# Performance work log

Hardware: AMD Instinct MI355X
Metric: run time of the kernel (lower is better)

The kernel has to match this reference:

```python
import jax, jax.numpy as jnp
import numpy as np


def setup_inputs() -> dict:
    key = jax.random.key(0)
    ks = jax.random.split(key, 16)
    s = 0.02
    return {
        "video": jax.random.normal(ks[0], (256, 10, 7, 7, 512), jnp.float32),
        "audio": jax.random.normal(ks[1], (10, 256, 128), jnp.float32),
        "Wv1": jax.random.normal(ks[2], (512, 512), jnp.float32) * s,
        "bv1": jnp.zeros((512,), jnp.float32),
        "Wa1": jax.random.normal(ks[3], (512, 128), jnp.float32) * s,
        "ba1": jnp.zeros((512,), jnp.float32),
        "Wb": jax.random.normal(ks[4], (256, 512), jnp.float32) * s,
        "bb": jnp.zeros((256,), jnp.float32),
        "Wc": jax.random.normal(ks[5], (512, 256), jnp.float32) * s,
        "bc": jnp.zeros((512,), jnp.float32),
        "Wv2": jax.random.normal(ks[6], (256, 512), jnp.float32) * s,
        "bv2": jnp.zeros((256,), jnp.float32),
        "Wa2": jax.random.normal(ks[7], (256, 128), jnp.float32) * s,
        "ba2": jnp.zeros((256,), jnp.float32),
        "Ws": jax.random.normal(ks[8], (1, 256), jnp.float32) * s,
        "bs": jnp.zeros((1,), jnp.float32),
    }


def reference(video, audio, Wv1, bv1, Wa1, ba1, Wb, bb, Wc, bc, Wv2, bv2, Wa2, ba2, Ws, bs):
    # video: [B, T, H, W, 512]; audio: [T, B, 128] (transposed inside, as in torch code)
    relu = jax.nn.relu
    audio = jnp.transpose(audio, (1, 0, 2))                  # [B, T, 128]
    B, T, H, W, Vd = video.shape
    BT, HW = B * T, H * W
    af = audio.reshape(BT, -1)                               # [BT, 128]
    vf = video.reshape(B, T, HW, Vd)                         # raw visual feature

    # channel attention
    aq1 = relu(af @ Wa1.T + ba1)[:, None, :]                 # [BT, 1, 512]
    vq1 = relu(vf @ Wv1.T + bv1).reshape(BT, HW, -1)         # [BT, 49, 512]
    avq = jnp.mean(aq1 * vq1, axis=-2)                       # [BT, 512]
    avq = relu(avq @ Wb.T + bb)                              # [BT, 256]
    c_att_maps = jax.nn.sigmoid(avq @ Wc.T + bc).reshape(B, T, 1, Vd)
    c_att = (vf * (c_att_maps + 1.0)).reshape(BT, HW, Vd)    # [BT, 49, 512]

    # spatial attention
    cq = relu(c_att @ Wv2.T + bv2)                           # [BT, 49, 256]
    aq2 = relu(af @ Wa2.T + ba2)[:, None, :]                 # [BT, 1, 256]
    logits = jnp.tanh((cq * aq2) @ Ws.T + bs)                # [BT, 49, 1]
    s_att = jax.nn.softmax(jnp.transpose(logits, (0, 2, 1)), axis=-1)  # [BT, 1, 49]

    out = jnp.matmul(s_att, c_att)                           # [BT, 1, 512]
    return out.reshape(B, T, Vd)
```

## Files before the change

### kernel.cpp

```cpp
#include <hip/hip_runtime.h>

typedef __bf16 bf16x8 __attribute__((ext_vector_type(8)));
typedef float f32x4 __attribute__((ext_vector_type(4)));

__device__ __forceinline__ unsigned short f2bf(float f) {
    union { float f; unsigned int u; } x; x.f = f;
    unsigned int r = x.u + 0x7FFFu + ((x.u >> 16) & 1u);
    return (unsigned short)(r >> 16);
}
__device__ __forceinline__ float bf2f(unsigned short v) {
    union { unsigned int u; float f; } x; x.u = ((unsigned int)v) << 16; return x.f;
}
__device__ __forceinline__ unsigned int cvt_pk_bf16(float lo, float hi) {
    unsigned int r;
    asm("v_cvt_pk_bf16_f32 %0, %1, %2" : "=v"(r) : "v"(lo), "v"(hi));
    return r;
}
__device__ __forceinline__ void async16(const void* g, void* l) {
    __builtin_amdgcn_global_load_lds(
        (const __attribute__((address_space(1))) unsigned int*)g,
        (__attribute__((address_space(3))) unsigned int*)l, 16, 0, 0);
}

__global__ __launch_bounds__(256) void k_front(
    const float* __restrict__ Wv1, const float* __restrict__ Wv2,
    unsigned short* __restrict__ Wv1bf, unsigned short* __restrict__ Wv2bf,
    const float* __restrict__ audio,
    const float* __restrict__ Wa1, const float* __restrict__ ba1,
    const float* __restrict__ Wa2, const float* __restrict__ ba2,
    float* __restrict__ aq1, float* __restrict__ aq2)
{
    const int b = blockIdx.x;
    const int tid = threadIdx.x;
    if (b < 384) {
        int base = b * 1024 + tid;
#pragma unroll
        for (int r = 0; r < 4; ++r) {
            int idx = base + r * 256;
            if (idx < 262144) Wv1bf[idx] = f2bf(Wv1[idx]);
            else              Wv2bf[idx - 262144] = f2bf(Wv2[idx - 262144]);
        }
        return;
    }
    __shared__ float afs[4][128];
    const int btBase = (b - 384) * 4;
    for (int i = tid; i < 512; i += 256) {
        int g = i >> 7, k = i & 127;
        int bt = btBase + g;
        int bb_ = bt / 10, t = bt - bb_ * 10;
        afs[g][k] = audio[(t * 256 + bb_) * 128 + k];
    }
    __syncthreads();
    const int c = tid;
    float a1a[4] = {0.f,0.f,0.f,0.f}, a1b[4] = {0.f,0.f,0.f,0.f}, a2[4] = {0.f,0.f,0.f,0.f};
    const float* w1a = Wa1 + c * 128;
    const float* w1b = Wa1 + (c + 256) * 128;
    const float* w2p = Wa2 + c * 128;
    for (int kk = 0; kk < 32; ++kk) {
        float4 va = *(const float4*)(w1a + kk * 4);
        float4 vb = *(const float4*)(w1b + kk * 4);
        float4 vc = *(const float4*)(w2p + kk * 4);
        float fa[4] = {va.x, va.y, va.z, va.w};
        float fb[4] = {vb.x, vb.y, vb.z, vb.w};
        float fc[4] = {vc.x, vc.y, vc.z, vc.w};
#pragma unroll
        for (int j = 0; j < 4; ++j) {
            int k = kk * 4 + j;
#pragma unroll
            for (int g = 0; g < 4; ++g) {
                float a = afs[g][k];
                a1a[g] += a * fa[j];
                a1b[g] += a * fb[j];
                a2[g]  += a * fc[j];
            }
        }
    }
    float b1a = ba1[c], b1b = ba1[c + 256], b2 = ba2[c];
#pragma unroll
    for (int g = 0; g < 4; ++g) {
        int bt = btBase + g;
        aq1[bt * 512 + c]       = fmaxf(a1a[g] + b1a, 0.f);
        aq1[bt * 512 + c + 256] = fmaxf(a1b[g] + b1b, 0.f);
        aq2[bt * 256 + c]       = fmaxf(a2[g] + b2, 0.f);
    }
}

__global__ __launch_bounds__(512) void k_chanatt_g(
    const float* __restrict__ video,
    const unsigned short* __restrict__ Wv1bf, const float* __restrict__ bv1,
    const float* __restrict__ aq1, float* __restrict__ avq)
{
    __shared__ unsigned short lds[2 * 12288];
    const int tid = threadIdx.x;
    const int wave = tid >> 6, lane = tid & 63, quad = lane >> 4, l16 = lane & 15;
    const int wm = wave >> 2, wn = wave & 3;
    const int mb = blockIdx.x >> 1, nb = blockIdx.x & 1;
    const int bt0 = mb * 2;

    const int arow = tid >> 2, ac = tid & 3;
    const int ahw = arow & 63, abtl = arow >> 6;
    const bool aok = (ahw < 49);
    const int aswz = (ac ^ (arow & 3)) << 3;
    const float* avsrc = video + (size_t)(bt0 + abtl) * 25088 + ahw * 512;
    float4 va, vb;

    auto aload = [&](int kt) {
        if (aok) {
            int k0 = kt * 32 + aswz;
            va = *(const float4*)(avsrc + k0);
            vb = *(const float4*)(avsrc + k0 + 4);
        }
    };
    auto awrite = [&](int buf) {
        if (aok) {
            uint4 o;
            o.x = cvt_pk_bf16(va.x, va.y); o.y = cvt_pk_bf16(va.z, va.w);
            o.z = cvt_pk_bf16(vb.x, vb.y); o.w = cvt_pk_bf16(vb.z, vb.w);
            *(uint4*)&lds[buf * 12288 + tid * 8] = o;
        }
    };
    auto stageB = [&](int buf, int kt) {
#pragma unroll
        for (int rep = 0; rep < 2; ++rep) {
            int q = tid + rep * 512;
            int row = q >> 2, c = q & 3;
            async16(Wv1bf + (size_t)((nb << 8) + row) * 512
                          + kt * 32 + ((c ^ (row & 3)) << 3),
                    &lds[buf * 12288 + 4096 + q * 8]);
        }
    };

    f32x4 acc[4][4];
#pragma unroll
    for (int mt = 0; mt < 4; ++mt)
#pragma unroll
        for (int nt = 0; nt < 4; ++nt)
            acc[mt][nt] = (f32x4){0.f, 0.f, 0.f, 0.f};

    aload(0);
    stageB(0, 0);
    awrite(0);
    __syncthreads();

    for (int kt = 0; kt < 16; ++kt) {
        int cur = kt & 1;
        if (kt < 15) { aload(kt + 1); stageB(cur ^ 1, kt + 1); }
        const int cb = cur * 12288;
        bf16x8 af[4];
#pragma unroll
        for (int mt = 0; mt < 4; ++mt) {
            int row = wm * 64 + mt * 16 + l16;
            af[mt] = *(const bf16x8*)&lds[cb + row * 32 + ((quad ^ (row & 3)) << 3)];
        }
#pragma unroll
        for (int nt = 0; nt < 4; ++nt) {
            int rowb = wn * 64 + nt * 16 + l16;
            bf16x8 bfr = *(const bf16x8*)&lds[cb + 4096 + rowb * 32 + ((quad ^ (rowb & 3)) << 3)];
#pragma unroll
            for (int mt = 0; mt < 4; ++mt)
                acc[mt][nt] = __builtin_amdgcn_mfma_f32_16x16x32_bf16(
                    af[mt], bfr, acc[mt][nt], 0, 0, 0);
        }
        if (kt < 15) awrite(cur ^ 1);
        __syncthreads();
    }

    const int bt = bt0 + wm;
#pragma unroll
    for (int nt = 0; nt < 4; ++nt) {
        int n = nb * 256 + wn * 64 + nt * 16 + l16;
        float bias = bv1[n];
        float s = 0.f;
#pragma unroll
        for (int mt = 0; mt < 4; ++mt)
#pragma unroll
            for (int r = 0; r < 4; ++r)
                if (mt < 3 || (quad == 0 && r == 0))
                    s += fmaxf(acc[mt][nt][r] + bias, 0.f);
        s += __shfl_xor(s, 16, 64);
        s += __shfl_xor(s, 32, 64);
        if (quad == 0) {
            avq[bt * 512 + n] = aq1[bt * 512 + n] * (s * (1.f / 49.f));
        }
    }
}

__global__ __launch_bounds__(256) void k_mlp(
    const float* __restrict__ avq,
    const float* __restrict__ Wb, const float* __restrict__ bb,
    const float* __restrict__ Wc, const float* __restrict__ bc,
    float* __restrict__ cmul)
{
    __shared__ float av[4][512];
    __shared__ float hid[4][256];
    const int btBase = blockIdx.x * 4;
    const int tid = threadIdx.x;
    for (int i = tid; i < 2048; i += 256) {
        int g = i >> 9, c = i & 511;
        av[g][c] = avq[(btBase + g) * 512 + c];
    }
    __syncthreads();
    {
        float a[4] = {0.f,0.f,0.f,0.f};
        const float* wrow = Wb + tid * 512;
        for (int kk = 0; kk < 128; ++kk) {
            float4 v = *(const float4*)(wrow + kk * 4);
            float w[4] = {v.x, v.y, v.z, v.w};
#pragma unroll
            for (int j = 0; j < 4; ++j)
#pragma unroll
                for (int g = 0; g < 4; ++g)
                    a[g] += av[g][kk * 4 + j] * w[j];
        }
        float bias = bb[tid];
#pragma unroll
        for (int g = 0; g < 4; ++g) hid[g][tid] = fmaxf(a[g] + bias, 0.f);
    }
    __syncthreads();
#pragma unroll
    for (int rep = 0; rep < 2; ++rep) {
        int c = tid + rep * 256;
        float a[4] = {0.f,0.f,0.f,0.f};
        const float* wrow = Wc + c * 256;
        for (int kk = 0; kk < 64; ++kk) {
            float4 v = *(const float4*)(wrow + kk * 4);
            float w[4] = {v.x, v.y, v.z, v.w};
#pragma unroll
            for (int j = 0; j < 4; ++j)
#pragma unroll
                for (int g = 0; g < 4; ++g)
                    a[g] += hid[g][kk * 4 + j] * w[j];
        }
        float bias = bc[c];
#pragma unroll
        for (int g = 0; g < 4; ++g) {
            float s = 1.f / (1.f + __expf(-(a[g] + bias)));
            cmul[(btBase + g) * 512 + c] = 1.f + s;
        }
    }
}

__global__ __launch_bounds__(512) void k_sgemm(
    const float* __restrict__ video,
    const float* __restrict__ cmul, const float* __restrict__ aq2,
    const unsigned short* __restrict__ Wv2bf, const float* __restrict__ bv2,
    const float* __restrict__ Wsp, const float* __restrict__ bsp,
    float* __restrict__ out)
{
    __shared__ unsigned short lds[2 * 12288];
    __shared__ float zsh[8][64];
    __shared__ float smloc[2][64];
    const int tid = threadIdx.x;
    const int wave = tid >> 6, lane = tid & 63, quad = lane >> 4, l16 = lane & 15;
    const int wm = wave >> 2, wn = wave & 3;
    const int bt0 = blockIdx.x * 2;

    const int arow = tid >> 2, ac = tid & 3;
    const int ahw = arow & 63, abtl = arow >> 6;
    const bool aok = (ahw < 49);
    const int aswz = (ac ^ (arow & 3)) << 3;
    const float* avsrc = video + (size_t)(bt0 + abtl) * 25088 + ahw * 512;
    const float* acm = cmul + (bt0 + abtl) * 512;
    float4 va, vb;
    float4 c0reg, c1reg;

    auto aload = [&](int kt) {
        if (aok) {
            int k0 = kt * 32 + aswz;
            va = *(const float4*)(avsrc + k0);
            vb = *(const float4*)(avsrc + k0 + 4);
            c0reg = *(const float4*)(acm + k0);
            c1reg = *(const float4*)(acm + k0 + 4);
        }
    };
    auto awrite = [&](int buf) {
        if (aok) {
            uint4 o;
            o.x = cvt_pk_bf16(va.x * c0reg.x, va.y * c0reg.y);
            o.y = cvt_pk_bf16(va.z * c0reg.z, va.w * c0reg.w);
            o.z = cvt_pk_bf16(vb.x * c1reg.x, vb.y * c1reg.y);
            o.w = cvt_pk_bf16(vb.z * c1reg.z, vb.w * c1reg.w);
            *(uint4*)&lds[buf * 12288 + tid * 8] = o;
        }
    };
    auto stageB = [&](int buf, int kt) {
#pragma unroll
        for (int rep = 0; rep < 2; ++rep) {
            int q = tid + rep * 512;
            int row = q >> 2, c = q & 3;
            async16(Wv2bf + (size_t)row * 512 + kt * 32 + ((c ^ (row & 3)) << 3),
                    &lds[buf * 12288 + 4096 + q * 8]);
        }
    };

    f32x4 acc[4][4];
#pragma unroll
    for (int mt = 0; mt < 4; ++mt)
#pragma unroll
        for (int nt = 0; nt < 4; ++nt)
            acc[mt][nt] = (f32x4){0.f, 0.f, 0.f, 0.f};

    aload(0);
    stageB(0, 0);
    awrite(0);
    __syncthreads();

    for (int kt = 0; kt < 16; ++kt) {
        int cur = kt & 1;
        if (kt < 15) { aload(kt + 1); stageB(cur ^ 1, kt + 1); }
        const int cb = cur * 12288;
        bf16x8 af[4];
#pragma unroll
        for (int mt = 0; mt < 4; ++mt) {
            int row = wm * 64 + mt * 16 + l16;
            af[mt] = *(const bf16x8*)&lds[cb + row * 32 + ((quad ^ (row & 3)) << 3)];
        }
#pragma unroll
        for (int nt = 0; nt < 4; ++nt) {
            int rowb = wn * 64 + nt * 16 + l16;
            bf16x8 bfr = *(const bf16x8*)&lds[cb + 4096 + rowb * 32 + ((quad ^ (rowb & 3)) << 3)];
#pragma unroll
            for (int mt = 0; mt < 4; ++mt)
                acc[mt][nt] = __builtin_amdgcn_mfma_f32_16x16x32_bf16(
                    af[mt], bfr, acc[mt][nt], 0, 0, 0);
        }
        if (kt < 15) awrite(cur ^ 1);
        __syncthreads();
    }

    const int bt = bt0 + wm;
    float zp[16];
#pragma unroll
    for (int i = 0; i < 16; ++i) zp[i] = 0.f;
#pragma unroll
    for (int nt = 0; nt < 4; ++nt) {
        int n = wn * 64 + nt * 16 + l16;
        float bias = bv2[n];
        float co = aq2[bt * 256 + n] * Wsp[n];
#pragma unroll
        for (int mt = 0; mt < 4; ++mt)
#pragma unroll
            for (int r = 0; r < 4; ++r)
                zp[mt * 4 + r] += fmaxf(acc[mt][nt][r] + bias, 0.f) * co;
    }
#pragma unroll
    for (int i = 0; i < 16; ++i) {
        float v = zp[i];
        v += __shfl_xor(v, 1, 64);
        v += __shfl_xor(v, 2, 64);
        v += __shfl_xor(v, 4, 64);
        v += __shfl_xor(v, 8, 64);
        zp[i] = v;
    }
    if (l16 == 0) {
#pragma unroll
        for (int mt = 0; mt < 4; ++mt)
#pragma unroll
            for (int r = 0; r < 4; ++r)
                zsh[wave][mt * 16 + quad * 4 + r] = zp[mt * 4 + r];
    }
    __syncthreads();

    if (wn == 0) {
        int hw = lane;
        float z = zsh[wm * 4 + 0][hw] + zsh[wm * 4 + 1][hw]
                + zsh[wm * 4 + 2][hw] + zsh[wm * 4 + 3][hw] + bsp[0];
        float t = tanhf(z);
        float v = (hw < 49) ? t : -1e30f;
#pragma unroll
        for (int off = 32; off; off >>= 1) v = fmaxf(v, __shfl_xor(v, off, 64));
        float e = (hw < 49) ? __expf(t - v) : 0.f;
        float se = e;
#pragma unroll
        for (int off = 32; off; off >>= 1) se += __shfl_xor(se, off, 64);
        smloc[wm][hw] = (hw < 49) ? (e / se) : 0.f;
    }
    __syncthreads();

    {
        int g = tid >> 2, part = tid & 3;
        int btl = g >> 6, cg = g & 63;
        const float* vs = video + (size_t)(bt0 + btl) * 25088 + cg * 8;
        float s[8];
#pragma unroll
        for (int j = 0; j < 8; ++j) s[j] = 0.f;
        for (int hw = part; hw < 49; hw += 4) {
            float w = smloc[btl][hw];
            float4 v0 = *(const float4*)(vs + hw * 512);
            float4 v1 = *(const float4*)(vs + hw * 512 + 4);
            s[0] += w * v0.x; s[1] += w * v0.y;
            s[2] += w * v0.z; s[3] += w * v0.w;
            s[4] += w * v1.x; s[5] += w * v1.y;
            s[6] += w * v1.z; s[7] += w * v1.w;
        }
#pragma unroll
        for (int j = 0; j < 8; ++j) {
            s[j] += __shfl_xor(s[j], 1, 64);
            s[j] += __shfl_xor(s[j], 2, 64);
        }
        if (part == 0) {
            const float* cm = cmul + (bt0 + btl) * 512 + cg * 8;
            float4 m0 = *(const float4*)cm;
            float4 m1 = *(const float4*)(cm + 4);
            float mm[8] = {m0.x, m0.y, m0.z, m0.w, m1.x, m1.y, m1.z, m1.w};
            float* op = out + (bt0 + btl) * 512 + cg * 8;
#pragma unroll
            for (int j = 0; j < 8; ++j) op[j] = s[j] * mm[j];
        }
    }
}

__global__ __launch_bounds__(256) void k_prep(
    const float* __restrict__ Wv1, const float* __restrict__ Wv2,
    unsigned short* __restrict__ Wv1bf, unsigned short* __restrict__ Wv2bf)
{
    int idx = blockIdx.x * 256 + threadIdx.x;
    if (idx < 262144) {
        Wv1bf[idx] = f2bf(Wv1[idx]);
    } else {
        int j = idx - 262144;
        Wv2bf[j] = f2bf(Wv2[j]);
    }
}

__global__ __launch_bounds__(256) void k_audio(
    const float* __restrict__ audio,
    const float* __restrict__ Wa1, const float* __restrict__ ba1,
    const float* __restrict__ Wa2, const float* __restrict__ ba2,
    float* __restrict__ aq1, float* __restrict__ aq2)
{
    __shared__ float afs[4][128];
    const int btBase = blockIdx.x * 4;
    const int tid = threadIdx.x;
    for (int i = tid; i < 512; i += 256) {
        int g = i >> 7, k = i & 127;
        int bt = btBase + g;
        int b = bt / 10, t = bt - b * 10;
        afs[g][k] = audio[(t * 256 + b) * 128 + k];
    }
    __syncthreads();
    const int c = tid;
    float a1a[4] = {0.f,0.f,0.f,0.f}, a1b[4] = {0.f,0.f,0.f,0.f}, a2[4] = {0.f,0.f,0.f,0.f};
    const float* w1a = Wa1 + c * 128;
    const float* w1b = Wa1 + (c + 256) * 128;
    const float* w2p = Wa2 + c * 128;
    for (int kk = 0; kk < 32; ++kk) {
        float4 va = *(const float4*)(w1a + kk * 4);
        float4 vb = *(const float4*)(w1b + kk * 4);
        float4 vc = *(const float4*)(w2p + kk * 4);
        float fa[4] = {va.x, va.y, va.z, va.w};
        float fb[4] = {vb.x, vb.y, vb.z, vb.w};
        float fc[4] = {vc.x, vc.y, vc.z, vc.w};
#pragma unroll
        for (int j = 0; j < 4; ++j) {
            int k = kk * 4 + j;
#pragma unroll
            for (int g = 0; g < 4; ++g) {
                float a = afs[g][k];
                a1a[g] += a * fa[j];
                a1b[g] += a * fb[j];
                a2[g]  += a * fc[j];
            }
        }
    }
    float b1a = ba1[c], b1b = ba1[c + 256], b2 = ba2[c];
#pragma unroll
    for (int g = 0; g < 4; ++g) {
        int bt = btBase + g;
        aq1[bt * 512 + c]       = fmaxf(a1a[g] + b1a, 0.f);
        aq1[bt * 512 + c + 256] = fmaxf(a1b[g] + b1b, 0.f);
        aq2[bt * 256 + c]       = fmaxf(a2[g] + b2, 0.f);
    }
}

__global__ __launch_bounds__(256) void k_chanatt_fb(
    const float* __restrict__ video,
    const unsigned short* __restrict__ Wv1bf, const float* __restrict__ bv1,
    const float* __restrict__ aq1, float* __restrict__ avq)
{
    __shared__ unsigned short At[49 * 512];
    const int bt = blockIdx.x;
    const int tid = threadIdx.x;
    const int wave = tid >> 6, lane = tid & 63, quad = lane >> 4, l16 = lane & 15;
    const float* vsrc = video + (size_t)bt * 25088;

    for (int c = tid; c < 3136; c += 256) {
        int row = c >> 6, ch = c & 63;
        float4 a = *(const float4*)(vsrc + row * 512 + ch * 8);
        float4 b = *(const float4*)(vsrc + row * 512 + ch * 8 + 4);
        float f[8] = {a.x, a.y, a.z, a.w, b.x, b.y, b.z, b.w};
        unsigned int o[8];
#pragma unroll
        for (int j = 0; j < 8; ++j) o[j] = f2bf(f[j]);
        uint4 pack;
        pack.x = o[0] | (o[1] << 16); pack.y = o[2] | (o[3] << 16);
        pack.z = o[4] | (o[5] << 16); pack.w = o[6] | (o[7] << 16);
        int chs = ch ^ (row & 7);
        *(uint4*)(&At[row * 512 + chs * 8]) = pack;
    }
    __syncthreads();

    f32x4 acc[4][8];
#pragma unroll
    for (int mt = 0; mt < 4; ++mt)
#pragma unroll
        for (int nt = 0; nt < 8; ++nt)
            acc[mt][nt] = (f32x4){0.f, 0.f, 0.f, 0.f};

    for (int kk = 0; kk < 16; ++kk) {
        int chunk = kk * 4 + quad;
        bf16x8 afrag[4];
#pragma unroll
        for (int mt = 0; mt < 4; ++mt) {
            int m = ((mt == 3) ? 33 : mt * 16) + l16;
            int chs = chunk ^ (m & 7);
            afrag[mt] = *(const bf16x8*)(&At[m * 512 + chs * 8]);
        }
        int koff = chunk * 8;
#pragma unroll
        for (int nt = 0; nt < 8; ++nt) {
            int n = (wave * 8 + nt) * 16 + l16;
            bf16x8 bfrag = *(const bf16x8*)(Wv1bf + n * 512 + koff);
#pragma unroll
            for (int mt = 0; mt < 4; ++mt)
                acc[mt][nt] = __builtin_amdgcn_mfma_f32_16x16x32_bf16(
                    afrag[mt], bfrag, acc[mt][nt], 0, 0, 0);
        }
    }

#pragma unroll
    for (int nt = 0; nt < 8; ++nt) {
        int n = (wave * 8 + nt) * 16 + l16;
        float bias = bv1[n];
        float s = 0.f;
#pragma unroll
        for (int mt = 0; mt < 4; ++mt)
#pragma unroll
            for (int r = 0; r < 4; ++r)
                if (mt < 3 || (quad == 3 && r == 3))
                    s += fmaxf(acc[mt][nt][r] + bias, 0.f);
        s += __shfl_xor(s, 16, 64);
        s += __shfl_xor(s, 32, 64);
        if (quad == 0) {
            float vm = s * (1.f / 49.f);
            avq[bt * 512 + n] = aq1[bt * 512 + n] * vm;
        }
    }
}

__global__ __launch_bounds__(256) void k_spatial_fb(
    const float* __restrict__ video,
    const float* __restrict__ cmul, const float* __restrict__ aq2,
    const unsigned short* __restrict__ Wv2bf, const float* __restrict__ bv2,
    const float* __restrict__ Wsp, const float* __restrict__ bsp,
    float* __restrict__ out)
{
    __shared__ unsigned short Ct[49 * 512];
    __shared__ float w2[256];
    __shared__ float zbuf[4][64];
    __shared__ float smwl[64];
    const int bt = blockIdx.x;
    const int tid = threadIdx.x;
    const int wave = tid >> 6, lane = tid & 63, quad = lane >> 4, l16 = lane & 15;
    const float* vsrc = video + (size_t)bt * 25088;
    const float* cm = cmul + bt * 512;

    for (int c = tid; c < 3136; c += 256) {
        int row = c >> 6, ch = c & 63;
        float4 a = *(const float4*)(vsrc + row * 512 + ch * 8);
        float4 b = *(const float4*)(vsrc + row * 512 + ch * 8 + 4);
        float f[8] = {a.x, a.y, a.z, a.w, b.x, b.y, b.z, b.w};
        float4 m0 = *(const float4*)(cm + ch * 8);
        float4 m1 = *(const float4*)(cm + ch * 8 + 4);
        float mm[8] = {m0.x, m0.y, m0.z, m0.w, m1.x, m1.y, m1.z, m1.w};
        unsigned int o[8];
#pragma unroll
        for (int j = 0; j < 8; ++j) o[j] = f2bf(f[j] * mm[j]);
        uint4 pack;
        pack.x = o[0] | (o[1] << 16); pack.y = o[2] | (o[3] << 16);
        pack.z = o[4] | (o[5] << 16); pack.w = o[6] | (o[7] << 16);
        int chs = ch ^ (row & 7);
        *(uint4*)(&Ct[row * 512 + chs * 8]) = pack;
    }
    w2[tid] = aq2[bt * 256 + tid] * Wsp[tid];
    if (lane >= 49) zbuf[wave][lane] = 0.f;
    __syncthreads();

    f32x4 acc[4][4];
#pragma unroll
    for (int mt = 0; mt < 4; ++mt)
#pragma unroll
        for (int nt = 0; nt < 4; ++nt)
            acc[mt][nt] = (f32x4){0.f, 0.f, 0.f, 0.f};

    for (int kk = 0; kk < 16; ++kk) {
        int chunk = kk * 4 + quad;
        bf16x8 afrag[4];
#pragma unroll
        for (int mt = 0; mt < 4; ++mt) {
            int m = ((mt == 3) ? 33 : mt * 16) + l16;
            int chs = chunk ^ (m & 7);
            afrag[mt] = *(const bf16x8*)(&Ct[m * 512 + chs * 8]);
        }
        int koff = chunk * 8;
#pragma unroll
        for (int nt = 0; nt < 4; ++nt) {
            int n = (wave * 4 + nt) * 16 + l16;
            bf16x8 bfrag = *(const bf16x8*)(Wv2bf + n * 512 + koff);
#pragma unroll
            for (int mt = 0; mt < 4; ++mt)
                acc[mt][nt] = __builtin_amdgcn_mfma_f32_16x16x32_bf16(
                    afrag[mt], bfrag, acc[mt][nt], 0, 0, 0);
        }
    }

    float zp[16];
#pragma unroll
    for (int i = 0; i < 16; ++i) zp[i] = 0.f;
#pragma unroll
    for (int nt = 0; nt < 4; ++nt) {
        int n = (wave * 4 + nt) * 16 + l16;
        float bias = bv2[n];
        float wnc = w2[n];
#pragma unroll
        for (int mt = 0; mt < 4; ++mt)
#pragma unroll
            for (int r = 0; r < 4; ++r)
                zp[mt * 4 + r] += fmaxf(acc[mt][nt][r] + bias, 0.f) * wnc;
    }
#pragma unroll
    for (int i = 0; i < 16; ++i) {
        float v = zp[i];
        v += __shfl_xor(v, 1, 64);
        v += __shfl_xor(v, 2, 64);
        v += __shfl_xor(v, 4, 64);
        v += __shfl_xor(v, 8, 64);
        zp[i] = v;
    }
    if (l16 == 0) {
#pragma unroll
        for (int mt = 0; mt < 4; ++mt)
#pragma unroll
            for (int r = 0; r < 4; ++r)
                if (mt < 3 || (quad == 3 && r == 3)) {
                    int row = ((mt == 3) ? 33 : mt * 16) + quad * 4 + r;
                    zbuf[wave][row] = zp[mt * 4 + r];
                }
    }
    __syncthreads();

    if (wave == 0) {
        int hw = lane;
        float z = zbuf[0][hw] + zbuf[1][hw] + zbuf[2][hw] + zbuf[3][hw] + bsp[0];
        float t = tanhf(z);
        float v = (hw < 49) ? t : -1e30f;
#pragma unroll
        for (int off = 32; off; off >>= 1) v = fmaxf(v, __shfl_xor(v, off, 64));
        float e = (hw < 49) ? __expf(t - v) : 0.f;
        float se = e;
#pragma unroll
        for (int off = 32; off; off >>= 1) se += __shfl_xor(se, off, 64);
        smwl[hw] = e / se;
    }
    __syncthreads();

#pragma unroll
    for (int rep = 0; rep < 2; ++rep) {
        int cidx = tid + rep * 256;
        int chb = cidx >> 3, jj = cidx & 7;
        float s = 0.f;
        for (int hw = 0; hw < 49; ++hw) {
            int chs = chb ^ (hw & 7);
            s += smwl[hw] * bf2f(Ct[hw * 512 + chs * 8 + jj]);
        }
        out[bt * 512 + cidx] = s;
    }
}

extern "C" void kernel_launch(void* const* d_in, const int* in_sizes, int n_in,
                              void* d_out, int out_size, void* d_ws, size_t ws_size,
                              hipStream_t stream) {
    const float* video = (const float*)d_in[0];
    const float* audio = (const float*)d_in[1];
    const float* Wv1 = (const float*)d_in[2];
    const float* bv1 = (const float*)d_in[3];
    const float* Wa1 = (const float*)d_in[4];
    const float* ba1 = (const float*)d_in[5];
    const float* Wb  = (const float*)d_in[6];
    const float* bb  = (const float*)d_in[7];
    const float* Wc  = (const float*)d_in[8];
    const float* bc  = (const float*)d_in[9];
    const float* Wv2 = (const float*)d_in[10];
    const float* bv2 = (const float*)d_in[11];
    const float* Wa2 = (const float*)d_in[12];
    const float* ba2 = (const float*)d_in[13];
    const float* Wsp = (const float*)d_in[14];
    const float* bsp = (const float*)d_in[15];
    float* out = (float*)d_out;

    const size_t NEED = 19136512u;
    if (ws_size >= NEED) {
        unsigned short* Wv1bf = (unsigned short*)d_ws;
        unsigned short* Wv2bf = Wv1bf + 262144;
        float* fbase = (float*)(Wv2bf + 131072);
        float* aq1  = fbase;
        float* aq2  = aq1 + 1310720;
        float* avq  = aq2 + 655360;
        float* cmul = avq + 1310720;

        k_front<<<1024, 256, 0, stream>>>(Wv1, Wv2, Wv1bf, Wv2bf,
                                          audio, Wa1, ba1, Wa2, ba2, aq1, aq2);
        k_chanatt_g<<<2560, 512, 0, stream>>>(video, Wv1bf, bv1, aq1, avq);
        k_mlp<<<640, 256, 0, stream>>>(avq, Wb, bb, Wc, bc, cmul);
        k_sgemm<<<1280, 512, 0, stream>>>(video, cmul, aq2, Wv2bf, bv2, Wsp, bsp, out);
    } else {
        float* ws = (float*)d_ws;
        float* aq1  = ws;
        float* aq2  = aq1 + 1310720;
        float* avq  = aq2 + 655360;
        float* cmul = avq + 1310720;
        unsigned short* Wv1bf = (unsigned short*)(cmul + 1310720);
        unsigned short* Wv2bf = Wv1bf + 262144;

        k_prep<<<1536, 256, 0, stream>>>(Wv1, Wv2, Wv1bf, Wv2bf);
        k_audio<<<640, 256, 0, stream>>>(audio, Wa1, ba1, Wa2, ba2, aq1, aq2);
        k_chanatt_fb<<<2560, 256, 0, stream>>>(video, Wv1bf, bv1, aq1, avq);
        k_mlp<<<640, 256, 0, stream>>>(avq, Wb, bb, Wc, bc, cmul);
        k_spatial_fb<<<2560, 256, 0, stream>>>(video, cmul, aq2, Wv2bf, bv2, Wsp, bsp, out);
    }
}
```

Baseline: 712.2 us.

## Deepen A-operand register prefetch to two stages and change LDS swizzle

In both GEMM kernels the video (A) tile global loads are now prefetched two k-steps ahead, using two register sets in a manually unrolled loop of two k-steps per iteration. The goal is to hide global load latency behind more MFMA work. The LDS XOR swizzle now keys on (row>>1)&3 instead of row&3, to reduce bank conflicts on the 16-byte fragment reads. The cost is higher register pressure from the doubled prefetch registers, which at 512 threads could cause spills.

Result: no change. 717.4 us (+0.7%).

```diff
diff --git a/kernel.cpp b/kernel.cpp
--- a/kernel.cpp
+++ b/kernel.cpp
@@ -100,22 +100,37 @@
     const int arow = tid >> 2, ac = tid & 3;
     const int ahw = arow & 63, abtl = arow >> 6;
     const bool aok = (ahw < 49);
-    const int aswz = (ac ^ (arow & 3)) << 3;
+    const int aswz = (ac ^ ((arow >> 1) & 3)) << 3;
     const float* avsrc = video + (size_t)(bt0 + abtl) * 25088 + ahw * 512;
-    float4 va, vb;
-
-    auto aload = [&](int kt) {
+    float4 vaA, vbA, vaB, vbB;
+
+    auto aloadA = [&](int kt) {
         if (aok) {
             int k0 = kt * 32 + aswz;
-            va = *(const float4*)(avsrc + k0);
-            vb = *(const float4*)(avsrc + k0 + 4);
-        }
-    };
-    auto awrite = [&](int buf) {
+            vaA = *(const float4*)(avsrc + k0);
+            vbA = *(const float4*)(avsrc + k0 + 4);
+        }
+    };
+    auto aloadB = [&](int kt) {
+        if (aok) {
+            int k0 = kt * 32 + aswz;
+            vaB = *(const float4*)(avsrc + k0);
+            vbB = *(const float4*)(avsrc + k0 + 4);
+        }
+    };
+    auto awriteA = [&](int buf) {
         if (aok) {
             uint4 o;
-            o.x = cvt_pk_bf16(va.x, va.y); o.y = cvt_pk_bf16(va.z, va.w);
-            o.z = cvt_pk_bf16(vb.x, vb.y); o.w = cvt_pk_bf16(vb.z, vb.w);
+            o.x = cvt_pk_bf16(vaA.x, vaA.y); o.y = cvt_pk_bf16(vaA.z, vaA.w);
+            o.z = cvt_pk_bf16(vbA.x, vbA.y); o.w = cvt_pk_bf16(vbA.z, vbA.w);
+            *(uint4*)&lds[buf * 12288 + tid * 8] = o;
+        }
+    };
+    auto awriteB = [&](int buf) {
+        if (aok) {
+            uint4 o;
+            o.x = cvt_pk_bf16(vaB.x, vaB.y); o.y = cvt_pk_bf16(vaB.z, vaB.w);
+            o.z = cvt_pk_bf16(vbB.x, vbB.y); o.w = cvt_pk_bf16(vbB.z, vbB.w);
             *(uint4*)&lds[buf * 12288 + tid * 8] = o;
         }
     };
@@ -125,7 +140,7 @@
             int q = tid + rep * 512;
             int row = q >> 2, c = q & 3;
             async16(Wv1bf + (size_t)((nb << 8) + row) * 512
-                          + kt * 32 + ((c ^ (row & 3)) << 3),
+                          + kt * 32 + ((c ^ ((row >> 1) & 3)) << 3),
                     &lds[buf * 12288 + 4096 + q * 8]);
         }
     };
@@ -137,31 +152,41 @@
         for (int nt = 0; nt < 4; ++nt)
             acc[mt][nt] = (f32x4){0.f, 0.f, 0.f, 0.f};
 
-    aload(0);
-    stageB(0, 0);
-    awrite(0);
-    __syncthreads();
-
-    for (int kt = 0; kt < 16; ++kt) {
-        int cur = kt & 1;
-        if (kt < 15) { aload(kt + 1); stageB(cur ^ 1, kt + 1); }
-        const int cb = cur * 12288;
+    auto compute = [&](int buf) {
+        const int cb = buf * 12288;
         bf16x8 af[4];
 #pragma unroll
         for (int mt = 0; mt < 4; ++mt) {
             int row = wm * 64 + mt * 16 + l16;
-            af[mt] = *(const bf16x8*)&lds[cb + row * 32 + ((quad ^ (row & 3)) << 3)];
+            af[mt] = *(const bf16x8*)&lds[cb + row * 32 + ((quad ^ ((row >> 1) & 3)) << 3)];
         }
 #pragma unroll
         for (int nt = 0; nt < 4; ++nt) {
             int rowb = wn * 64 + nt * 16 + l16;
-            bf16x8 bfr = *(const bf16x8*)&lds[cb + 4096 + rowb * 32 + ((quad ^ (rowb & 3)) << 3)];
+            bf16x8 bfr = *(const bf16x8*)&lds[cb + 4096 + rowb * 32
+                                              + ((quad ^ ((rowb >> 1) & 3)) << 3)];
 #pragma unroll
             for (int mt = 0; mt < 4; ++mt)
                 acc[mt][nt] = __builtin_amdgcn_mfma_f32_16x16x32_bf16(
                     af[mt], bfr, acc[mt][nt], 0, 0, 0);
         }
-        if (kt < 15) awrite(cur ^ 1);
+    };
+
+    aloadA(0); awriteA(0);
+    aloadB(1);
+    stageB(0, 0);
+    __syncthreads();
+
+    for (int kt2 = 0; kt2 < 16; kt2 += 2) {
+        stageB(1, kt2 + 1);
+        if (kt2 + 2 < 16) aloadA(kt2 + 2);
+        compute(0);
+        awriteB(1);
+        __syncthreads();
+        if (kt2 + 2 < 16) stageB(0, kt2 + 2);
+        if (kt2 + 3 < 16) aloadB(kt2 + 3);
+        compute(1);
+        if (kt2 + 2 < 16) awriteA(0);
         __syncthreads();
     }
 
@@ -258,28 +283,47 @@
     const int arow = tid >> 2, ac = tid & 3;
     const int ahw = arow & 63, abtl = arow >> 6;
     const bool aok = (ahw < 49);
-    const int aswz = (ac ^ (arow & 3)) << 3;
+    const int aswz = (ac ^ ((arow >> 1) & 3)) << 3;
     const float* avsrc = video + (size_t)(bt0 + abtl) * 25088 + ahw * 512;
     const float* acm = cmul + (bt0 + abtl) * 512;
-    float4 va, vb;
-    float4 c0reg, c1reg;
-
-    auto aload = [&](int kt) {
+    float4 vaA, vbA, c0A, c1A;
+    float4 vaB, vbB, c0B, c1B;
+
+    auto aloadA = [&](int kt) {
         if (aok) {
             int k0 = kt * 32 + aswz;
-            va = *(const float4*)(avsrc + k0);
-            vb = *(const float4*)(avsrc + k0 + 4);
-            c0reg = *(const float4*)(acm + k0);
-            c1reg = *(const float4*)(acm + k0 + 4);
-        }
-    };
-    auto awrite = [&](int buf) {
+            vaA = *(const float4*)(avsrc + k0);
+            vbA = *(const float4*)(avsrc + k0 + 4);
+            c0A = *(const float4*)(acm + k0);
+            c1A = *(const float4*)(acm + k0 + 4);
+        }
+    };
+    auto aloadB = [&](int kt) {
+        if (aok) {
+            int k0 = kt * 32 + aswz;
+            vaB = *(const float4*)(avsrc + k0);
+            vbB = *(const float4*)(avsrc + k0 + 4);
+            c0B = *(const float4*)(acm + k0);
+            c1B = *(const float4*)(acm + k0 + 4);
+        }
+    };
+    auto awriteA = [&](int buf) {
         if (aok) {
             uint4 o;
-            o.x = cvt_pk_bf16(va.x * c0reg.x, va.y * c0reg.y);
-            o.y = cvt_pk_bf16(va.z * c0reg.z, va.w * c0reg.w);
-            o.z = cvt_pk_bf16(vb.x * c1reg.x, vb.y * c1reg.y);
-            o.w = cvt_pk_bf16(vb.z * c1reg.z, vb.w * c1reg.w);
+            o.x = cvt_pk_bf16(vaA.x * c0A.x, vaA.y * c0A.y);
+            o.y = cvt_pk_bf16(vaA.z * c0A.z, vaA.w * c0A.w);
+            o.z = cvt_pk_bf16(vbA.x * c1A.x, vbA.y * c1A.y);
+            o.w = cvt_pk_bf16(vbA.z * c1A.z, vbA.w * c1A.w);
+            *(uint4*)&lds[buf * 12288 + tid * 8] = o;
+        }
+    };
+    auto awriteB = [&](int buf) {
+        if (aok) {
+            uint4 o;
+            o.x = cvt_pk_bf16(vaB.x * c0B.x, vaB.y * c0B.y);
+            o.y = cvt_pk_bf16(vaB.z * c0B.z, vaB.w * c0B.w);
+            o.z = cvt_pk_bf16(vbB.x * c1B.x, vbB.y * c1B.y);
+            o.w = cvt_pk_bf16(vbB.z * c1B.z, vbB.w * c1B.w);
             *(uint4*)&lds[buf * 12288 + tid * 8] = o;
         }
     };
@@ -288,7 +332,7 @@
         for (int rep = 0; rep < 2; ++rep) {
             int q = tid + rep * 512;
             int row = q >> 2, c = q & 3;
-            async16(Wv2bf + (size_t)row * 512 + kt * 32 + ((c ^ (row & 3)) << 3),
+            async16(Wv2bf + (size_t)row * 512 + kt * 32 + ((c ^ ((row >> 1) & 3)) << 3),
                     &lds[buf * 12288 + 4096 + q * 8]);
         }
     };
@@ -300,31 +344,41 @@
         for (int nt = 0; nt < 4; ++nt)
             acc[mt][nt] = (f32x4){0.f, 0.f, 0.f, 0.f};
 
-    aload(0);
-    stageB(0, 0);
-    awrite(0);
-    __syncthreads();
-
-    for (int kt = 0; kt < 16; ++kt) {
-        int cur = kt & 1;
-        if (kt < 15) { aload(kt + 1); stageB(cur ^ 1, kt + 1); }
-        const int cb = cur * 12288;
+    auto compute = [&](int buf) {
+        const int cb = buf * 12288;
         bf16x8 af[4];
 #pragma unroll
         for (int mt = 0; mt < 4; ++mt) {
             int row = wm * 64 + mt * 16 + l16;
-            af[mt] = *(const bf16x8*)&lds[cb + row * 32 + ((quad ^ (row & 3)) << 3)];
+            af[mt] = *(const bf16x8*)&lds[cb + row * 32 + ((quad ^ ((row >> 1) & 3)) << 3)];
         }
 #pragma unroll
         for (int nt = 0; nt < 4; ++nt) {
             int rowb = wn * 64 + nt * 16 + l16;
-            bf16x8 bfr = *(const bf16x8*)&lds[cb + 4096 + rowb * 32 + ((quad ^ (rowb & 3)) << 3)];
+            bf16x8 bfr = *(const bf16x8*)&lds[cb + 4096 + rowb * 32
+                                              + ((quad ^ ((rowb >> 1) & 3)) << 3)];
 #pragma unroll
             for (int mt = 0; mt < 4; ++mt)
                 acc[mt][nt] = __builtin_amdgcn_mfma_f32_16x16x32_bf16(
                     af[mt], bfr, acc[mt][nt], 0, 0, 0);
         }
-        if (kt < 15) awrite(cur ^ 1);
+    };
+
+    aloadA(0); awriteA(0);
+    aloadB(1);
+    stageB(0, 0);
+    __syncthreads();
+
+    for (int kt2 = 0; kt2 < 16; kt2 += 2) {
+        stageB(1, kt2 + 1);
+        if (kt2 + 2 < 16) aloadA(kt2 + 2);
+        compute(0);
+        awriteB(1);
+        __syncthreads();
+        if (kt2 + 2 < 16) stageB(0, kt2 + 2);
+        if (kt2 + 3 < 16) aloadB(kt2 + 3);
+        compute(1);
+        if (kt2 + 2 < 16) awriteA(0);
         __syncthreads();
     }
 
```
